# Optimization experiments

Hardware: AMD Instinct MI355X
Metric: run time of the kernel (lower is better)

The kernel has to match this reference:

```python
import jax, jax.numpy as jnp
import numpy as np

B, C, H, W = 16, 64, 257, 257  # H, W odd so low/high subband shapes match


def _dw(x, filt, stride):
    """Depthwise conv2d: x [B,C,h,w], filt [1,1,kh,kw] broadcast to all C channels."""
    c = x.shape[1]
    k = jnp.broadcast_to(filt, (c, 1) + filt.shape[2:])  # [C,1,kh,kw]
    return jax.lax.conv_general_dilated(
        x, k, window_strides=stride, padding='VALID',
        feature_group_count=c,
        dimension_numbers=('NCHW', 'OIHW', 'NCHW'))


def setup_inputs() -> dict:
    key = jax.random.key(0)
    kx, k1, k2, k3, k4 = jax.random.split(key, 5)
    return {
        'x': jax.random.normal(kx, (B, C, H, W), dtype=jnp.float32),
        'low_h': jax.random.uniform(k1, (1, 1, 1, 2), dtype=jnp.float32),
        'high_h': jax.random.uniform(k2, (1, 1, 1, 2), dtype=jnp.float32),
        'low_v': jax.random.uniform(k3, (1, 1, 2, 1), dtype=jnp.float32),
        'high_v': jax.random.uniform(k4, (1, 1, 2, 1), dtype=jnp.float32),
    }


def reference(x, low_h, high_h, low_v, high_v):
    # kernel_size == 2 -> all reflect pads in the torch code are zero-width no-ops.
    # Horizontal lifting: even-phase (low) from x, odd-phase (high) from x shifted by 1.
    x_l = _dw(x, low_h, (1, 2))                 # [B,C,H,W//2]   (W odd -> (W-1)//2... = 128)
    x_h = _dw(x[:, :, :, 1:], high_h, (1, 2))   # [B,C,H,128]
    # Vertical lifting on each horizontal band.
    x_ll = _dw(x_l, low_v, (2, 1))              # [B,C,128,128]
    x_hl = _dw(x_l[:, :, 1:, :], high_v, (2, 1))
    x_lh = _dw(x_h, low_v, (2, 1))
    x_hh = _dw(x_h[:, :, 1:, :], high_v, (2, 1))
    return jnp.concatenate([x_ll, x_hl, x_lh, x_hh], axis=1)  # [B,4C,128,128]
```

## Files before the change

kernel.cpp:

```cpp
#include <hip/hip_runtime.h>


#define B_ 16
#define C_ 64
#define H_ 257
#define W_ 257
#define HO_ 128
#define WO_ 128
#define SEGS 4
#define SEG_ROWS (HO_ / SEGS)

__global__ __launch_bounds__(256) void ldw_down_kernel(
    const float* __restrict__ x,
    const float* __restrict__ low_h,
    const float* __restrict__ high_h,
    const float* __restrict__ low_v,
    const float* __restrict__ high_v,
    float* __restrict__ out)
{
    const float lh0 = low_h[0],  lh1 = low_h[1];
    const float hh0 = high_h[0], hh1 = high_h[1];
    const float lv0 = low_v[0],  lv1 = low_v[1];
    const float hv0 = high_v[0], hv1 = high_v[1];

    const int tid = blockIdx.x * blockDim.x + threadIdx.x;
    const int wo  = tid & (WO_ - 1);
    const int seg = (tid >> 7) & (SEGS - 1);
    const int p   = tid >> 9;
    if (p >= B_ * C_) return;

    const long PLANE_IN = (long)H_ * W_;
    const float* xin = x + (long)p * PLANE_IN;

    const int b = p >> 6;
    const int c = p & (C_ - 1);
    const long PLANE_OUT = (long)HO_ * WO_;
    float* oll = out + (long)b * (4 * C_) * PLANE_OUT + (long)c * PLANE_OUT + wo;
    float* ohl = oll + (long)C_ * PLANE_OUT;
    float* olh = oll + (long)(2 * C_) * PLANE_OUT;
    float* ohh = oll + (long)(3 * C_) * PLANE_OUT;

    const int ho0 = seg * SEG_ROWS;
    const int col = 2 * wo;

    {
        const float* r0 = xin + (long)(2 * ho0) * W_ + col;
        float a0 = r0[0], a1 = r0[1], a2 = r0[2];
        float xl0 = lh0 * a0 + lh1 * a1;
        float xh0 = hh0 * a1 + hh1 * a2;

        #pragma unroll 4
        for (int i = 0; i < SEG_ROWS; ++i) {
            const int ho = ho0 + i;
            const float* r1 = xin + (long)(2 * ho + 1) * W_ + col;
            const float* r2 = r1 + W_;
            const float b0 = r1[0], b1 = r1[1], b2 = r1[2];
            const float c0 = r2[0], c1 = r2[1], c2 = r2[2];

            const float xl1 = lh0 * b0 + lh1 * b1;
            const float xh1 = hh0 * b1 + hh1 * b2;
            const float xl2 = lh0 * c0 + lh1 * c1;
            const float xh2 = hh0 * c1 + hh1 * c2;

            const long o = (long)ho * WO_;
            oll[o] = lv0 * xl0 + lv1 * xl1;
            ohl[o] = hv0 * xl1 + hv1 * xl2;
            olh[o] = lv0 * xh0 + lv1 * xh1;
            ohh[o] = hv0 * xh1 + hv1 * xh2;

            xl0 = xl2;
            xh0 = xh2;
        }
    }
}

extern "C" void kernel_launch(void* const* d_in, const int* in_sizes, int n_in,
                              void* d_out, int out_size, void* d_ws, size_t ws_size,
                              hipStream_t stream) {
    const float* x      = (const float*)d_in[0];
    const float* low_h  = (const float*)d_in[1];
    const float* high_h = (const float*)d_in[2];
    const float* low_v  = (const float*)d_in[3];
    const float* high_v = (const float*)d_in[4];
    float* out = (float*)d_out;

    const int total_threads = B_ * C_ * WO_ * SEGS;
    const int block = 256;
    const int grid = (total_threads + block - 1) / block;
    ldw_down_kernel<<<grid, block, 0, stream>>>(x, low_h, high_h, low_v, high_v, out);
}
```

Before: 468.5 us.

## Vectorize loads and stores with 4 outputs per thread and one block per plane

```diff
diff --git a/kernel.cpp b/kernel.cpp
--- a/kernel.cpp
+++ b/kernel.cpp
@@ -7,8 +7,88 @@
 #define W_ 257
 #define HO_ 128
 #define WO_ 128
-#define SEGS 4
+#define SEGS 8
 #define SEG_ROWS (HO_ / SEGS)
+#define NP (B_ * C_)
+
+typedef float f32x4 __attribute__((ext_vector_type(4)));
+
+template<int PAR>
+__device__ __forceinline__ void load9(const float* __restrict__ rp, float* a) {
+    if constexpr (PAR == 0) {
+        float2 v0 = *reinterpret_cast<const float2*>(rp + 0);
+        float2 v1 = *reinterpret_cast<const float2*>(rp + 2);
+        float2 v2 = *reinterpret_cast<const float2*>(rp + 4);
+        float2 v3 = *reinterpret_cast<const float2*>(rp + 6);
+        a[0] = v0.x; a[1] = v0.y; a[2] = v1.x; a[3] = v1.y;
+        a[4] = v2.x; a[5] = v2.y; a[6] = v3.x; a[7] = v3.y;
+        a[8] = rp[8];
+    } else {
+        a[0] = rp[0];
+        float2 v0 = *reinterpret_cast<const float2*>(rp + 1);
+        float2 v1 = *reinterpret_cast<const float2*>(rp + 3);
+        float2 v2 = *reinterpret_cast<const float2*>(rp + 5);
+        float2 v3 = *reinterpret_cast<const float2*>(rp + 7);
+        a[1] = v0.x; a[2] = v0.y; a[3] = v1.x; a[4] = v1.y;
+        a[5] = v2.x; a[6] = v2.y; a[7] = v3.x; a[8] = v3.y;
+    }
+}
+
+template<int PE>
+__device__ __forceinline__ void run_seg(
+    const float* __restrict__ row0,
+    float* __restrict__ o_ll,
+    float lh0, float lh1, float hh0, float hh1,
+    float lv0, float lv1, float hv0, float hv1)
+{
+    const long BAND = (long)C_ * HO_ * WO_;
+    float* o_hl = o_ll + BAND;
+    float* o_lh = o_ll + 2 * BAND;
+    float* o_hh = o_ll + 3 * BAND;
+
+    float a[9];
+    load9<PE>(row0, a);
+    float xl0[4], xh0[4];
+    #pragma unroll
+    for (int j = 0; j < 4; ++j) {
+        xl0[j] = lh0 * a[2 * j]     + lh1 * a[2 * j + 1];
+        xh0[j] = hh0 * a[2 * j + 1] + hh1 * a[2 * j + 2];
+    }
+
+    const float* rp = row0 + W_;
+
+    #pragma unroll 4
+    for (int i = 0; i < SEG_ROWS; ++i) {
+        float bb[9], cc[9];
+        load9<PE ^ 1>(rp, bb);
+        load9<PE>(rp + W_, cc);
+        rp += 2 * W_;
+
+        float ll[4], hl[4], lhv[4], hh[4];
+        #pragma unroll
+        for (int j = 0; j < 4; ++j) {
+            const float xl1 = lh0 * bb[2 * j]     + lh1 * bb[2 * j + 1];
+            const float xh1 = hh0 * bb[2 * j + 1] + hh1 * bb[2 * j + 2];
+            const float xl2 = lh0 * cc[2 * j]     + lh1 * cc[2 * j + 1];
+            const float xh2 = hh0 * cc[2 * j + 1] + hh1 * cc[2 * j + 2];
+            ll[j]  = lv0 * xl0[j] + lv1 * xl1;
+            hl[j]  = hv0 * xl1    + hv1 * xl2;
+            lhv[j] = lv0 * xh0[j] + lv1 * xh1;
+            hh[j]  = hv0 * xh1    + hv1 * xh2;
+            xl0[j] = xl2;
+            xh0[j] = xh2;
+        }
+        f32x4 vll = {ll[0], ll[1], ll[2], ll[3]};
+        f32x4 vhl = {hl[0], hl[1], hl[2], hl[3]};
+        f32x4 vlh = {lhv[0], lhv[1], lhv[2], lhv[3]};
+        f32x4 vhh = {hh[0], hh[1], hh[2], hh[3]};
+        __builtin_nontemporal_store(vll, reinterpret_cast<f32x4*>(o_ll));
+        __builtin_nontemporal_store(vhl, reinterpret_cast<f32x4*>(o_hl));
+        __builtin_nontemporal_store(vlh, reinterpret_cast<f32x4*>(o_lh));
+        __builtin_nontemporal_store(vhh, reinterpret_cast<f32x4*>(o_hh));
+        o_ll += WO_; o_hl += WO_; o_lh += WO_; o_hh += WO_;
+    }
+}
 
 __global__ __launch_bounds__(256) void ldw_down_kernel(
     const float* __restrict__ x,
@@ -23,55 +103,24 @@
     const float lv0 = low_v[0],  lv1 = low_v[1];
     const float hv0 = high_v[0], hv1 = high_v[1];
 
-    const int tid = blockIdx.x * blockDim.x + threadIdx.x;
-    const int wo  = tid & (WO_ - 1);
-    const int seg = (tid >> 7) & (SEGS - 1);
-    const int p   = tid >> 9;
-    if (p >= B_ * C_) return;
-
-    const long PLANE_IN = (long)H_ * W_;
-    const float* xin = x + (long)p * PLANE_IN;
+    const int p   = blockIdx.x;
+    const int t   = threadIdx.x;
+    const int wt  = t & 31;
+    const int seg = t >> 5;
 
     const int b = p >> 6;
     const int c = p & (C_ - 1);
-    const long PLANE_OUT = (long)HO_ * WO_;
-    float* oll = out + (long)b * (4 * C_) * PLANE_OUT + (long)c * PLANE_OUT + wo;
-    float* ohl = oll + (long)C_ * PLANE_OUT;
-    float* olh = oll + (long)(2 * C_) * PLANE_OUT;
-    float* ohh = oll + (long)(3 * C_) * PLANE_OUT;
+    const int ho0 = seg * SEG_ROWS;
 
-    const int ho0 = seg * SEG_ROWS;
-    const int col = 2 * wo;
+    const float* row0 = x + (long)p * (H_ * W_) + (long)(2 * ho0) * W_ + 8 * wt;
+    float* o_ll = out + (long)b * (4 * C_) * (HO_ * WO_)
+                      + (long)c * (HO_ * WO_)
+                      + (long)ho0 * WO_ + 4 * wt;
 
-    {
-        const float* r0 = xin + (long)(2 * ho0) * W_ + col;
-        float a0 = r0[0], a1 = r0[1], a2 = r0[2];
-        float xl0 = lh0 * a0 + lh1 * a1;
-        float xh0 = hh0 * a1 + hh1 * a2;
-
-        #pragma unroll 4
-        for (int i = 0; i < SEG_ROWS; ++i) {
-            const int ho = ho0 + i;
-            const float* r1 = xin + (long)(2 * ho + 1) * W_ + col;
-            const float* r2 = r1 + W_;
-            const float b0 = r1[0], b1 = r1[1], b2 = r1[2];
-            const float c0 = r2[0], c1 = r2[1], c2 = r2[2];
-
-            const float xl1 = lh0 * b0 + lh1 * b1;
-            const float xh1 = hh0 * b1 + hh1 * b2;
-            const float xl2 = lh0 * c0 + lh1 * c1;
-            const float xh2 = hh0 * c1 + hh1 * c2;
-
-            const long o = (long)ho * WO_;
-            oll[o] = lv0 * xl0 + lv1 * xl1;
-            ohl[o] = hv0 * xl1 + hv1 * xl2;
-            olh[o] = lv0 * xh0 + lv1 * xh1;
-            ohh[o] = hv0 * xh1 + hv1 * xh2;
-
-            xl0 = xl2;
-            xh0 = xh2;
-        }
-    }
+    if ((p & 1) == 0)
+        run_seg<0>(row0, o_ll, lh0, lh1, hh0, hh1, lv0, lv1, hv0, hv1);
+    else
+        run_seg<1>(row0, o_ll, lh0, lh1, hh0, hh1, lv0, lv1, hv0, hv1);
 }
 
 extern "C" void kernel_launch(void* const* d_in, const int* in_sizes, int n_in,
@@ -84,8 +133,5 @@
     const float* high_v = (const float*)d_in[4];
     float* out = (float*)d_out;
 
-    const int total_threads = B_ * C_ * WO_ * SEGS;
-    const int block = 256;
-    const int grid = (total_threads + block - 1) / block;
-    ldw_down_kernel<<<grid, block, 0, stream>>>(x, low_h, high_h, low_v, high_v, out);
+    ldw_down_kernel<<<NP, 256, 0, stream>>>(x, low_h, high_h, low_v, high_v, out);
 }
```

Result: no change. 471.2 us (+0.6%).

## Stage input rows through an LDS ring buffer with coalesced loads per slab

Applied to the files above, without the earlier changes.

```diff
diff --git a/kernel.cpp b/kernel.cpp
--- a/kernel.cpp
+++ b/kernel.cpp
@@ -7,10 +7,12 @@
 #define W_ 257
 #define HO_ 128
 #define WO_ 128
-#define SEGS 4
-#define SEG_ROWS (HO_ / SEGS)
+#define OROWS 16
+#define SLABS (HO_ / OROWS)
+#define PADW 264
+#define NSLOT 8
 
-__global__ __launch_bounds__(256) void ldw_down_kernel(
+__global__ __launch_bounds__(256, 8) void ldw_down_kernel(
     const float* __restrict__ x,
     const float* __restrict__ low_h,
     const float* __restrict__ high_h,
@@ -18,59 +20,96 @@
     const float* __restrict__ high_v,
     float* __restrict__ out)
 {
+    __shared__ float lds[NSLOT * PADW];
+
     const float lh0 = low_h[0],  lh1 = low_h[1];
     const float hh0 = high_h[0], hh1 = high_h[1];
     const float lv0 = low_v[0],  lv1 = low_v[1];
     const float hv0 = high_v[0], hv1 = high_v[1];
 
-    const int tid = blockIdx.x * blockDim.x + threadIdx.x;
-    const int wo  = tid & (WO_ - 1);
-    const int seg = (tid >> 7) & (SEGS - 1);
-    const int p   = tid >> 9;
-    if (p >= B_ * C_) return;
+    const int bid  = blockIdx.x;
+    const int p    = bid >> 3;
+    const int slab = bid & (SLABS - 1);
+    const int ho0  = slab * OROWS;
 
-    const long PLANE_IN = (long)H_ * W_;
-    const float* xin = x + (long)p * PLANE_IN;
+    const int t    = threadIdx.x;
+    const int wave = t >> 6;
+    const int lane = t & 63;
+    const int wo   = t & 127;
+    const int orow = t >> 7;
+
+    const float* xrow0 = x + (long)p * (H_ * W_) + (long)(2 * ho0) * W_;
 
     const int b = p >> 6;
     const int c = p & (C_ - 1);
-    const long PLANE_OUT = (long)HO_ * WO_;
-    float* oll = out + (long)b * (4 * C_) * PLANE_OUT + (long)c * PLANE_OUT + wo;
-    float* ohl = oll + (long)C_ * PLANE_OUT;
-    float* olh = oll + (long)(2 * C_) * PLANE_OUT;
-    float* ohh = oll + (long)(3 * C_) * PLANE_OUT;
+    const long BAND = (long)C_ * HO_ * WO_;
+    float* o_ll = out + (long)b * 4 * BAND + (long)c * (HO_ * WO_);
+    float* o_hl = o_ll + BAND;
+    float* o_lh = o_ll + 2 * BAND;
+    float* o_hh = o_ll + 3 * BAND;
 
-    const int ho0 = seg * SEG_ROWS;
-    const int col = 2 * wo;
+    #pragma unroll
+    for (int k = 0; k < 2; ++k) {
+        const int rel = wave + 4 * k;
+        const float* src = xrow0 + (long)rel * W_;
+        float* dst = &lds[(rel & (NSLOT - 1)) * PADW];
+        float v0 = src[lane];
+        float v1 = src[lane + 64];
+        float v2 = src[lane + 128];
+        float v3 = src[lane + 192];
+        dst[lane]       = v0;
+        dst[lane + 64]  = v1;
+        dst[lane + 128] = v2;
+        dst[lane + 192] = v3;
+        if (lane == 0) dst[256] = src[256];
+    }
+    __syncthreads();
 
-    {
-        const float* r0 = xin + (long)(2 * ho0) * W_ + col;
-        float a0 = r0[0], a1 = r0[1], a2 = r0[2];
-        float xl0 = lh0 * a0 + lh1 * a1;
-        float xh0 = hh0 * a1 + hh1 * a2;
+    #pragma unroll
+    for (int i = 0; i < 8; ++i) {
+        const int rel = 4 * i + 8 + wave;
+        const bool do_stage = (rel <= 32);
+        float v0, v1, v2, v3, vt;
+        const float* src = xrow0 + (long)rel * W_;
+        if (do_stage) {
+            v0 = src[lane];
+            v1 = src[lane + 64];
+            v2 = src[lane + 128];
+            v3 = src[lane + 192];
+            if (lane == 0) vt = src[256];
+        }
 
-        #pragma unroll 4
-        for (int i = 0; i < SEG_ROWS; ++i) {
-            const int ho = ho0 + i;
-            const float* r1 = xin + (long)(2 * ho + 1) * W_ + col;
-            const float* r2 = r1 + W_;
-            const float b0 = r1[0], b1 = r1[1], b2 = r1[2];
-            const float c0 = r2[0], c1 = r2[1], c2 = r2[2];
+        const int base = 4 * i + 2 * orow;
+        float xl[3], xh[3];
+        #pragma unroll
+        for (int r = 0; r < 3; ++r) {
+            const float* rp = &lds[((base + r) & (NSLOT - 1)) * PADW + 2 * wo];
+            const float2 f01 = *reinterpret_cast<const float2*>(rp);
+            const float  f2  = rp[2];
+            xl[r] = lh0 * f01.x + lh1 * f01.y;
+            xh[r] = hh0 * f01.y + hh1 * f2;
+        }
+        const float r_ll = lv0 * xl[0] + lv1 * xl[1];
+        const float r_hl = hv0 * xl[1] + hv1 * xl[2];
+        const float r_lh = lv0 * xh[0] + lv1 * xh[1];
+        const float r_hh = hv0 * xh[1] + hv1 * xh[2];
 
-            const float xl1 = lh0 * b0 + lh1 * b1;
-            const float xh1 = hh0 * b1 + hh1 * b2;
-            const float xl2 = lh0 * c0 + lh1 * c1;
-            const float xh2 = hh0 * c1 + hh1 * c2;
+        const long o = (long)(ho0 + 2 * i + orow) * WO_ + wo;
+        __builtin_nontemporal_store(r_ll, o_ll + o);
+        __builtin_nontemporal_store(r_hl, o_hl + o);
+        __builtin_nontemporal_store(r_lh, o_lh + o);
+        __builtin_nontemporal_store(r_hh, o_hh + o);
 
-            const long o = (long)ho * WO_;
-            oll[o] = lv0 * xl0 + lv1 * xl1;
-            ohl[o] = hv0 * xl1 + hv1 * xl2;
-            olh[o] = lv0 * xh0 + lv1 * xh1;
-            ohh[o] = hv0 * xh1 + hv1 * xh2;
-
-            xl0 = xl2;
-            xh0 = xh2;
+        __syncthreads();
+        if (do_stage) {
+            float* dst = &lds[(rel & (NSLOT - 1)) * PADW];
+            dst[lane]       = v0;
+            dst[lane + 64]  = v1;
+            dst[lane + 128] = v2;
+            dst[lane + 192] = v3;
+            if (lane == 0) dst[256] = vt;
         }
+        __syncthreads();
     }
 }
 
@@ -84,8 +123,6 @@
     const float* high_v = (const float*)d_in[4];
     float* out = (float*)d_out;
 
-    const int total_threads = B_ * C_ * WO_ * SEGS;
-    const int block = 256;
-    const int grid = (total_threads + block - 1) / block;
-    ldw_down_kernel<<<grid, block, 0, stream>>>(x, low_h, high_h, low_v, high_v, out);
+    const int grid = B_ * C_ * SLABS;
+    ldw_down_kernel<<<grid, 256, 0, stream>>>(x, low_h, high_h, low_v, high_v, out);
 }
```

New measurement: 467.8 us. About the same (-0.2%).
